# Kernel optimization log

Hardware: AMD Instinct MI355X
Metric: run time of the kernel (lower is better)

Reference implementation:

```python
import jax, jax.numpy as jnp
import numpy as np

IN, HID, OUT, HEADS = 64, 128, 256, 4
BL, N, E = 4, 2500, 120000
NT = BL * N  # total flattened nodes = 10000
NEG_SLOPE = 0.2  # PyG GATv2Conv default


def setup_inputs() -> dict:
    key = jax.random.key(0)
    ks = jax.random.split(key, 32)
    inp = {}
    inp["x"] = jax.random.normal(ks[0], (BL, N, IN), jnp.float32)
    inp["edge_index"] = jax.random.randint(ks[1], (2, E), 0, NT, jnp.int32)
    inp["edge_weight"] = jax.random.uniform(ks[2], (E, 1), jnp.float32)
    # layers: (fan_in, out_per_head, heads)
    dims = [(IN, HID, HEADS), (HID * HEADS, HID, HEADS), (HID * HEADS, OUT, 1)]
    i = 3
    for l, (fi, fo, h) in enumerate(dims):
        sc = 1.0 / np.sqrt(fi)
        inp[f"Wl{l}"] = jax.random.normal(ks[i], (fi, h * fo), jnp.float32) * sc
        inp[f"bl{l}"] = jax.random.normal(ks[i + 1], (h * fo,), jnp.float32) * 0.01
        inp[f"Wr{l}"] = jax.random.normal(ks[i + 2], (fi, h * fo), jnp.float32) * sc
        inp[f"br{l}"] = jax.random.normal(ks[i + 3], (h * fo,), jnp.float32) * 0.01
        inp[f"We{l}"] = jax.random.normal(ks[i + 4], (1, h * fo), jnp.float32)
        inp[f"att{l}"] = jax.random.normal(ks[i + 5], (h, fo), jnp.float32) / np.sqrt(fo)
        inp[f"bias{l}"] = jax.random.normal(ks[i + 6], (h * fo,), jnp.float32) * 0.01
        i += 7
    return inp


def _gat_layer(x, src, dst, ew, Wl, bl, Wr, br, We, att, bias):
    # x: (NT, F); ew: (E, 1); att: (H, C)
    H, C = att.shape
    n = x.shape[0]
    xl = (x @ Wl + bl).reshape(n, H, C)          # source transform
    xr = (x @ Wr + br).reshape(n, H, C)          # target transform
    xe = (ew @ We).reshape(-1, H, C)             # edge-attr transform (no bias in PyG lin_edge)
    e = jax.nn.leaky_relu(xl[src] + xr[dst] + xe, negative_slope=NEG_SLOPE)  # (E, H, C)
    logits = jnp.einsum('ehc,hc->eh', e, att)    # (E, H)
    # segment softmax over incoming edges of each destination node
    m = jax.lax.stop_gradient(jax.ops.segment_max(logits, dst, num_segments=n))
    m = jnp.where(jnp.isfinite(m), m, 0.0)
    p = jnp.exp(logits - m[dst])
    s = jax.ops.segment_sum(p, dst, num_segments=n)
    alpha = p / (s[dst] + 1e-16)                 # (E, H)
    msg = xl[src] * alpha[:, :, None]            # (E, H, C)
    out = jax.ops.segment_sum(msg, dst, num_segments=n)  # (NT, H, C)
    return out.reshape(n, H * C) + bias


def reference(x, edge_index, edge_weight,
              Wl0, bl0, Wr0, br0, We0, att0, bias0,
              Wl1, bl1, Wr1, br1, We1, att1, bias1,
              Wl2, bl2, Wr2, br2, We2, att2, bias2):
    bl_, n_, f_ = x.shape
    h = x.reshape(bl_ * n_, f_)
    src, dst = edge_index[0], edge_index[1]
    h = jax.nn.elu(_gat_layer(h, src, dst, edge_weight, Wl0, bl0, Wr0, br0, We0, att0, bias0))
    h = jax.nn.elu(_gat_layer(h, src, dst, edge_weight, Wl1, bl1, Wr1, br1, We1, att1, bias1))
    h = _gat_layer(h, src, dst, edge_weight, Wl2, bl2, Wr2, br2, We2, att2, bias2)
    return h.reshape(bl_, n_, -1)
```

## Files before the change

### kernel.cpp

```cpp
#include <hip/hip_runtime.h>
#include <hip/hip_bf16.h>
#include <math.h>

#define NT    10000
#define NE    120000
#define MP    10240

using h8    = __attribute__((ext_vector_type(8))) _Float16;
using h4    = __attribute__((ext_vector_type(4))) _Float16;
using f32x4 = __attribute__((ext_vector_type(4))) float;

struct Args {
    const float* x;
    const int*   src;
    const int*   dst;
    const float* ew;
    const float* W[6];
    const float* bl[3];
    const float* br[3];
    const float* We[3];
    const float* att[3];
    const float* bias[3];
    _Float16* wt[6];
    _Float16* xf;
    _Float16* xl;  _Float16* xr;
    _Float16* af;
    float* out;
    int* rowptr; int* cntcur; int* csr_src; float* csr_w;
};

__device__ __forceinline__ void gemm_jobs(
    const _Float16* __restrict__ A,
    const _Float16* __restrict__ WlT, const _Float16* __restrict__ WrT,
    const float* __restrict__ biasl, const float* __restrict__ biasr,
    _Float16* __restrict__ outl, _Float16* __restrict__ outr,
    int M, int N, int K, int njobs, int job0, int jstep, _Float16* sm)
{
    _Float16* sA = sm;
    _Float16* sB = sm + 8192;

    int tid = threadIdx.x;
    int wave = tid >> 6, lane = tid & 63;
    int lr15 = lane & 15;
    int lk8  = (lane >> 4) * 8;
    int fq = lane >> 4;
    int fc = lane & 15;
    int wm = (wave & 1) << 6;
    int wn = (wave >> 1) << 6;

    for (int job = job0; job < njobs; job += jstep) {
        int xcd = job & 7;
        int kk  = job >> 3;
        int r   = kk % 10;
        int byy = kk / 10;
        int bm  = (xcd * 10 + r) * 128;

        int nby = N >> 7;
        bool isR = byy >= nby;
        int bnn = (isR ? byy - nby : byy) << 7;
        const _Float16* Bh = isR ? WrT : WlT;
        const float* bias  = isR ? biasr : biasl;
        _Float16* out      = isR ? outr : outl;

        f32x4 acc[4][4] = {};

        for (int k0 = 0; k0 < K; k0 += 64) {
            __syncthreads();
            #pragma unroll
            for (int q = 0; q < 8; ++q) {
                int p = wave * 8 + q;
                int bufi = p >> 4;
                int c = p & 15;
                int sub = c >> 3, rg = c & 7;
                const _Float16* g = (bufi == 0) ? A : Bh;
                int rowbase = (bufi == 0) ? bm : bnn;
                _Float16* sb = sm + bufi * 8192 + c * 512;
                const _Float16* gp = g + (size_t)(rowbase + rg * 16 + lr15) * K
                                       + k0 + sub * 32 + lk8;
                __builtin_amdgcn_global_load_lds(
                    (const __attribute__((address_space(1))) void*)gp,
                    (__attribute__((address_space(3))) void*)sb,
                    16, 0, 0);
            }
            __syncthreads();

            #pragma unroll
            for (int sub = 0; sub < 2; ++sub) {
                h8 af[4];
                #pragma unroll
                for (int i = 0; i < 4; ++i) {
                    int c = sub * 8 + (wave & 1) * 4 + i;
                    af[i] = *(const h8*)(sA + c * 512 + lane * 8);
                }
                #pragma unroll
                for (int j = 0; j < 4; ++j) {
                    int c = sub * 8 + (wave >> 1) * 4 + j;
                    h8 bf = *(const h8*)(sB + c * 512 + lane * 8);
                    #pragma unroll
                    for (int i = 0; i < 4; ++i)
                        acc[i][j] = __builtin_amdgcn_mfma_f32_16x16x32_f16(af[i], bf, acc[i][j], 0, 0, 0);
                }
            }
        }

        #pragma unroll
        for (int j = 0; j < 4; ++j) {
            int col = bnn + wn + j * 16 + fc;
            float bv = bias[col];
            #pragma unroll
            for (int i = 0; i < 4; ++i) {
                int row0 = bm + wm + i * 16 + fq * 4;
                #pragma unroll
                for (int reg = 0; reg < 4; ++reg) {
                    int row = row0 + reg;
                    if (row < M)
                        out[(size_t)row * N + col] = (_Float16)(acc[i][j][reg] + bv);
                }
            }
        }
    }
}

__global__ void preph_k(Args a) {
    __shared__ float sf[32 * 33];
    const int mat_cum[7] = {0, 32, 64, 320, 576, 704, 832};
    const int mat_K[6]   = {64, 64, 512, 512, 512, 512};
    const int mat_N[6]   = {512, 512, 512, 512, 256, 256};
    int w = blockIdx.x;
    int tid = threadIdx.x;
    int tx = tid & 31, ty = tid >> 5;
    if (w < 832) {
        int t = w;
        int mm = 0;
        #pragma unroll
        for (int q = 1; q < 6; ++q) if (t >= mat_cum[q]) mm = q;
        int tt = t - mat_cum[mm];
        int K = mat_K[mm], N = mat_N[mm];
        int tiles_k = K >> 5;
        int tk = tt % tiles_k, tn = tt / tiles_k;
        const float* W = a.W[mm];
        _Float16* T = a.wt[mm];
        int bk = tk * 32, bn = tn * 32;
        #pragma unroll
        for (int i = 0; i < 4; ++i)
            sf[(ty * 4 + i) * 33 + tx] =
                W[(size_t)(bk + ty * 4 + i) * N + bn + tx];
        __syncthreads();
        #pragma unroll
        for (int i = 0; i < 4; ++i) {
            int nn = ty * 4 + i;
            T[(size_t)(bn + nn) * K + bk + tx] = (_Float16)sf[tx * 33 + nn];
        }
    } else {
        int i = (w - 832) * 1024 + tid * 4;
        float4 v = *(const float4*)(a.x + i);
        h4 o;
        o[0] = (_Float16)v.x; o[1] = (_Float16)v.y;
        o[2] = (_Float16)v.z; o[3] = (_Float16)v.w;
        *(h4*)(a.xf + i) = o;
    }
    for (int e = w * 256 + tid; e < NE; e += 1457 * 256)
        atomicAdd(&a.cntcur[a.dst[e]], 1);
}

__global__ __launch_bounds__(1024) void scan_k(Args a) {
    __shared__ int si[1024];
    int tid = threadIdx.x;
    const int PER = 10;
    int base = tid * PER;
    int s = 0;
    for (int i = 0; i < PER; ++i) {
        int idx = base + i;
        if (idx < NT) s += a.cntcur[idx];
    }
    si[tid] = s;
    __syncthreads();
    for (int off = 1; off < 1024; off <<= 1) {
        int v = (tid >= off) ? si[tid - off] : 0;
        __syncthreads();
        si[tid] += v;
        __syncthreads();
    }
    int run = (tid == 0) ? 0 : si[tid - 1];
    for (int i = 0; i < PER; ++i) {
        int idx = base + i;
        if (idx < NT) { a.rowptr[idx] = run; run += a.cntcur[idx]; }
        else if (idx == NT) a.rowptr[idx] = run;
    }
}

__global__ __launch_bounds__(256, 4) void scatgemm_k(Args a) {
    __shared__ __align__(16) _Float16 sm[2 * 8192];
    int b = blockIdx.x;
    if (b < 160) {
        int* cursor = a.cntcur + NT;
        for (int e = b * 256 + (int)threadIdx.x; e < NE; e += 160 * 256) {
            int d = a.dst[e];
            int pos = atomicAdd(&cursor[d], 1);
            int idx = a.rowptr[d] + pos;
            a.csr_src[idx] = a.src[e];
            a.csr_w[idx]  = a.ew[e];
        }
    } else {
        gemm_jobs(a.xf, a.wt[0], a.wt[1], a.bl[0], a.br[0],
                  a.xl, a.xr, NT, 512, 64, 640, b - 160, 640, sm);
    }
}

__global__ __launch_bounds__(256, 4) void gemm_k(
    const _Float16* A, const _Float16* WlT, const _Float16* WrT,
    const float* bl, const float* br,
    _Float16* ol, _Float16* orr, int M, int N, int K, int njobs) {
    __shared__ __align__(16) _Float16 sm[2 * 8192];
    gemm_jobs(A, WlT, WrT, bl, br, ol, orr, M, N, K, njobs,
              blockIdx.x, gridDim.x, sm);
}

template<int C, int H, int WPN, bool DO_ELU, bool FP16OUT>
__global__ __launch_bounds__(256) void edge_k(
    const _Float16* __restrict__ xl, const _Float16* __restrict__ xr,
    const int* __restrict__ rowptr, const int* __restrict__ csr_src,
    const float* __restrict__ csr_w,
    const float* __restrict__ We, const float* __restrict__ att,
    const float* __restrict__ bias,
    float* __restrict__ outf, _Float16* __restrict__ outh)
{
    constexpr int CHT = C * H;
    constexpr int CHW = CHT / WPN;
    constexpr int VPT = CHW / 64;
    constexpr int HW  = H / WPN;
    constexpr int G   = 64 / HW;

    int gw   = blockIdx.x * 4 + ((int)threadIdx.x >> 6);
    int node = gw / WPN;
    int wp   = gw % WPN;
    int lane = threadIdx.x & 63;
    if (node >= NT) return;
    int c0 = wp * CHW + lane * VPT;
    size_t nbase = (size_t)node * CHT + c0;

    float xr_reg[VPT], we_reg[VPT], att_reg[VPT];
    {
        _Float16 t[VPT];
        if (VPT == 8) *(h8*)t = *(const h8*)(xr + nbase);
        else          *(h4*)t = *(const h4*)(xr + nbase);
        #pragma unroll
        for (int v = 0; v < VPT; ++v) xr_reg[v] = (float)t[v];
    }
    #pragma unroll
    for (int v = 0; v < VPT; v += 4) {
        *(float4*)(we_reg + v)   = *(const float4*)(We + c0 + v);
        *(float4*)(att_reg + v)  = *(const float4*)(att + c0 + v);
    }

    int rs = rowptr[node];
    int re = rowptr[node + 1];

    float m = -INFINITY, ssum = 0.f;
    float av[VPT];
    #pragma unroll
    for (int v = 0; v < VPT; ++v) av[v] = 0.f;

    for (int base = rs; base < re; base += 64) {
        int cn = re - base;
        if (cn > 64) cn = 64;
        int le = base + lane;
        int cl = (le < re) ? le : (re - 1);
        int   sidx = csr_src[cl];
        float swt  = csr_w[cl];

        _Float16 r0[VPT], r1[VPT], r2[VPT], r3[VPT];
        auto ld = [&](int j, _Float16* dst) {
            int s = __shfl(sidx, j, 64);
            const _Float16* p = xl + (size_t)s * CHT + c0;
            if (VPT == 8) *(h8*)dst = *(const h8*)p;
            else          *(h4*)dst = *(const h4*)p;
        };
        auto step = [&](const _Float16* rc, int j) {
            float w = __shfl(swt, j, 64);
            float part = 0.f;
            #pragma unroll
            for (int v = 0; v < VPT; ++v) {
                float t = fmaf(w, we_reg[v], xr_reg[v]) + (float)rc[v];
                t = fmaxf(t, 0.2f * t);
                part += t * att_reg[v];
            }
            #pragma unroll
            for (int off = G / 2; off > 0; off >>= 1)
                part += __shfl_xor(part, off, 64);
            float newm = fmaxf(m, part);
            float fac = __expf(m - newm);
            float p = __expf(part - newm);
            ssum = ssum * fac + p;
            #pragma unroll
            for (int v = 0; v < VPT; ++v)
                av[v] = fmaf(av[v], fac, p * (float)rc[v]);
            m = newm;
        };

        ld(0, r0);
        if (cn > 1) ld(1, r1);
        if (cn > 2) ld(2, r2);
        if (cn > 3) ld(3, r3);

        int j = 0;
        while (j < cn) {
            step(r0, j);
            if (j + 4 < cn) ld(j + 4, r0);
            if (++j >= cn) break;
            step(r1, j);
            if (j + 4 < cn) ld(j + 4, r1);
            if (++j >= cn) break;
            step(r2, j);
            if (j + 4 < cn) ld(j + 4, r2);
            if (++j >= cn) break;
            step(r3, j);
            if (j + 4 < cn) ld(j + 4, r3);
            ++j;
        }
    }

    float inv = 1.f / (ssum + 1e-16f);
    #pragma unroll
    for (int v = 0; v < VPT; ++v) {
        float o = av[v] * inv + bias[c0 + v];
        if (DO_ELU) o = (o > 0.f) ? o : (__expf(o) - 1.f);
        if (FP16OUT) outh[nbase + v] = (_Float16)o;
        else         outf[nbase + v] = o;
    }
}

extern "C" void kernel_launch(void* const* d_in, const int* in_sizes, int n_in,
                              void* d_out, int out_size, void* d_ws, size_t ws_size,
                              hipStream_t stream) {
    Args a;
    a.x   = (const float*)d_in[0];
    const int* ei = (const int*)d_in[1];
    a.src = ei;
    a.dst = ei + NE;
    a.ew  = (const float*)d_in[2];
    for (int l = 0; l < 3; ++l) {
        int base = 3 + 7 * l;
        a.W[2 * l]     = (const float*)d_in[base + 0];
        a.bl[l]        = (const float*)d_in[base + 1];
        a.W[2 * l + 1] = (const float*)d_in[base + 2];
        a.br[l]        = (const float*)d_in[base + 3];
        a.We[l]        = (const float*)d_in[base + 4];
        a.att[l]       = (const float*)d_in[base + 5];
        a.bias[l]      = (const float*)d_in[base + 6];
    }

    size_t off = 0;
    auto alloc = [&](size_t bytes) -> void* {
        void* p = (char*)d_ws + off;
        off += (bytes + 255) & ~(size_t)255;
        return p;
    };
    a.xl   = (_Float16*)alloc((size_t)MP * 512 * 2);
    a.xr   = (_Float16*)alloc((size_t)MP * 512 * 2);
    a.af   = (_Float16*)alloc((size_t)MP * 512 * 2);
    a.xf   = (_Float16*)alloc((size_t)MP * 64 * 2);
    const int KD[3] = {64, 512, 512};
    const int ND[3] = {512, 512, 256};
    for (int l = 0; l < 3; ++l) {
        a.wt[2 * l]     = (_Float16*)alloc((size_t)KD[l] * ND[l] * 2);
        a.wt[2 * l + 1] = (_Float16*)alloc((size_t)KD[l] * ND[l] * 2);
    }
    a.rowptr  = (int*)alloc((size_t)(NT + 1) * 4);
    a.cntcur  = (int*)alloc((size_t)2 * NT * 4);
    a.csr_src = (int*)alloc((size_t)NE * 4);
    a.csr_w   = (float*)alloc((size_t)NE * 4);
    a.out     = (float*)d_out;

    hipMemsetAsync(a.cntcur, 0, (size_t)2 * NT * 4, stream);
    preph_k<<<1457, 256, 0, stream>>>(a);
    scan_k<<<1, 1024, 0, stream>>>(a);
    scatgemm_k<<<800, 256, 0, stream>>>(a);

    edge_k<128, 4, 2, true, true><<<5000, 256, 0, stream>>>(
        a.xl, a.xr, a.rowptr, a.csr_src, a.csr_w,
        a.We[0], a.att[0], a.bias[0], nullptr, a.af);

    gemm_k<<<640, 256, 0, stream>>>(a.af, a.wt[2], a.wt[3],
                                    a.bl[1], a.br[1], a.xl, a.xr,
                                    NT, 512, 512, 640);
    edge_k<128, 4, 2, true, true><<<5000, 256, 0, stream>>>(
        a.xl, a.xr, a.rowptr, a.csr_src, a.csr_w,
        a.We[1], a.att[1], a.bias[1], nullptr, a.af);

    gemm_k<<<320, 256, 0, stream>>>(a.af, a.wt[4], a.wt[5],
                                    a.bl[2], a.br[2], a.xl, a.xr,
                                    NT, 256, 512, 320);
    edge_k<256, 1, 1, false, false><<<2500, 256, 0, stream>>>(
        a.xl, a.xr, a.rowptr, a.csr_src, a.csr_w,
        a.We[2], a.att[2], a.bias[2], a.out, nullptr);
}
```

Before: 287.0 us.

## Double-buffer GEMM LDS tiles with K-step 32 and retune edge kernel grouping

The GEMM inner loop now stages 32-wide K slices into two alternating LDS buffers. The next slice's global-to-LDS load is issued before the current slice's MFMAs run, so memory latency overlaps with compute and one barrier per step is dropped. Separately, the first two edge kernels change a template parameter from 2 to 1 and launch half as many blocks. This presumably gives each block more nodes to process. The cost is more loop iterations in the GEMM, and the GEMM may race if the compiler does not wait for the async loads before the barrier.

```diff
diff --git a/kernel.cpp b/kernel.cpp
--- a/kernel.cpp
+++ b/kernel.cpp
@@ -36,9 +36,6 @@
     _Float16* __restrict__ outl, _Float16* __restrict__ outr,
     int M, int N, int K, int njobs, int job0, int jstep, _Float16* sm)
 {
-    _Float16* sA = sm;
-    _Float16* sB = sm + 8192;
-
     int tid = threadIdx.x;
     int wave = tid >> 6, lane = tid & 63;
     int lr15 = lane & 15;
@@ -64,42 +61,41 @@
 
         f32x4 acc[4][4] = {};
 
-        for (int k0 = 0; k0 < K; k0 += 64) {
-            __syncthreads();
-            #pragma unroll
-            for (int q = 0; q < 8; ++q) {
-                int p = wave * 8 + q;
-                int bufi = p >> 4;
-                int c = p & 15;
-                int sub = c >> 3, rg = c & 7;
+        auto stage = [&](int b, int k0) {
+            #pragma unroll
+            for (int q = 0; q < 4; ++q) {
+                int p = wave * 4 + q;
+                int bufi = p >> 3;
+                int rg = p & 7;
                 const _Float16* g = (bufi == 0) ? A : Bh;
                 int rowbase = (bufi == 0) ? bm : bnn;
-                _Float16* sb = sm + bufi * 8192 + c * 512;
+                _Float16* sb = sm + b * 8192 + bufi * 4096 + rg * 512;
                 const _Float16* gp = g + (size_t)(rowbase + rg * 16 + lr15) * K
-                                       + k0 + sub * 32 + lk8;
+                                       + k0 + lk8;
                 __builtin_amdgcn_global_load_lds(
                     (const __attribute__((address_space(1))) void*)gp,
                     (__attribute__((address_space(3))) void*)sb,
                     16, 0, 0);
             }
+        };
+
+        int nt = K >> 5;
+        stage(0, 0);
+        for (int t = 0; t < nt; ++t) {
             __syncthreads();
-
-            #pragma unroll
-            for (int sub = 0; sub < 2; ++sub) {
-                h8 af[4];
+            if (t + 1 < nt) stage((t + 1) & 1, (t + 1) << 5);
+            const _Float16* sA = sm + (t & 1) * 8192;
+            const _Float16* sB = sA + 4096;
+            h8 af[4];
+            #pragma unroll
+            for (int i = 0; i < 4; ++i)
+                af[i] = *(const h8*)(sA + ((wave & 1) * 4 + i) * 512 + lane * 8);
+            #pragma unroll
+            for (int j = 0; j < 4; ++j) {
+                h8 bf = *(const h8*)(sB + ((wave >> 1) * 4 + j) * 512 + lane * 8);
                 #pragma unroll
-                for (int i = 0; i < 4; ++i) {
-                    int c = sub * 8 + (wave & 1) * 4 + i;
-                    af[i] = *(const h8*)(sA + c * 512 + lane * 8);
-                }
-                #pragma unroll
-                for (int j = 0; j < 4; ++j) {
-                    int c = sub * 8 + (wave >> 1) * 4 + j;
-                    h8 bf = *(const h8*)(sB + c * 512 + lane * 8);
-                    #pragma unroll
-                    for (int i = 0; i < 4; ++i)
-                        acc[i][j] = __builtin_amdgcn_mfma_f32_16x16x32_f16(af[i], bf, acc[i][j], 0, 0, 0);
-                }
+                for (int i = 0; i < 4; ++i)
+                    acc[i][j] = __builtin_amdgcn_mfma_f32_16x16x32_f16(af[i], bf, acc[i][j], 0, 0, 0);
             }
         }
 
@@ -377,14 +373,14 @@
     scan_k<<<1, 1024, 0, stream>>>(a);
     scatgemm_k<<<800, 256, 0, stream>>>(a);
 
-    edge_k<128, 4, 2, true, true><<<5000, 256, 0, stream>>>(
+    edge_k<128, 4, 1, true, true><<<2500, 256, 0, stream>>>(
         a.xl, a.xr, a.rowptr, a.csr_src, a.csr_w,
         a.We[0], a.att[0], a.bias[0], nullptr, a.af);
 
     gemm_k<<<640, 256, 0, stream>>>(a.af, a.wt[2], a.wt[3],
                                     a.bl[1], a.br[1], a.xl, a.xr,
                                     NT, 512, 512, 640);
-    edge_k<128, 4, 2, true, true><<<5000, 256, 0, stream>>>(
+    edge_k<128, 4, 1, true, true><<<2500, 256, 0, stream>>>(
         a.xl, a.xr, a.rowptr, a.csr_src, a.csr_w,
         a.We[1], a.att[1], a.bias[1], nullptr, a.af);
 
```

Measured after the change: 277.6 us. -3.3%, faster.
